# Performance work log

Hardware: AMD Instinct MI355X
Metric: run time of the kernel (lower is better)

## Reference

```python
import jax, jax.numpy as jnp
import numpy as np

N = 100000
K = 8
S = 2048
E = 131072


def setup_inputs() -> dict:
    key = jax.random.key(0)
    k1, k2, k3, k4, k5, k6, k7 = jax.random.split(key, 7)
    return {
        "beta": jax.random.normal(k1, (N,), dtype=jnp.float32),
        "a": jax.random.normal(k2, (1,), dtype=jnp.float32),
        "Zp": jax.random.normal(k3, (K, N), dtype=jnp.float32),
        "Gp": jax.random.normal(k4, (N, K), dtype=jnp.float32),
        "sample_idx": jax.random.randint(k5, (S,), 0, N),
        "sparse_i": jax.random.randint(k6, (E,), 0, N),
        "sparse_j": jax.random.randint(k7, (E,), 0, N),
    }


def reference(beta, a, Zp, Gp, sample_idx, sparse_i, sparse_j):
    # Z: softmax over archetype dim k (dim=0 of [k, N])
    Z = jax.nn.softmax(Zp, axis=0)          # [k, N]
    G = jax.nn.sigmoid(Gp)                  # [N, k]
    ZtG = Z.T * G                           # [N, k]
    C = ZtG / ZtG.sum(axis=0)               # [N, k], column-normalized
    sp_a = jax.nn.softplus(a)               # [1]

    Zs = Z[:, sample_idx]                   # [k, S]
    Cs = C[sample_idx, :]                   # [S, k]
    beta_s = beta[sample_idx]               # [S]

    # non-edge term: all-pairs distances within the sample
    bpair = beta_s[:, None] + beta_s[None, :]          # [S, S]
    M = (Zs @ Cs @ Zs).T                               # [S, k]
    diff = M[:, None, :] - M[None, :, :] + 1e-06       # [S, S, k]
    dist = jnp.sqrt(jnp.sum(diff ** 2, axis=-1))       # [S, S]
    mat = jnp.exp(bpair - sp_a * dist)                 # [S, S]
    mat_nd = mat - jnp.diag(jnp.diagonal(mat))
    e_vec = jnp.exp(jnp.ones((S,), dtype=mat.dtype))   # faithful to torch.exp(ones)
    z_pdist1 = 0.5 * (e_vec @ (mat_nd @ e_vec))        # scalar

    # edge term over sampled edges
    M2 = Zs @ Cs                                       # [k, k]
    beta_e = beta[sparse_i] + beta[sparse_j]           # [E]
    di = (M2 @ Z[:, sparse_i]).T                       # [E, k]
    dj = (M2 @ Z[:, sparse_j]).T                       # [E, k]
    dd = di - dj + 1e-06                               # [E, k]
    z_pdist2 = jnp.sum(beta_e - sp_a * jnp.sqrt(jnp.sum(dd ** 2, axis=-1)))

    return z_pdist2 - z_pdist1
```

## Files before the change

### kernel.cpp

```cpp
#include <hip/hip_runtime.h>
#include <hip/hip_bf16.h>

#define N_NODES 100000
#define K_DIM   8
#define S_SAMP  2048
#define E_EDGE  131072

#define CS_BLOCKS 256
#define M2_BLOCKS 8

#define CS_PART_OFF   0
#define M2P_OFF       2048
#define SPA_OFF       2560
#define PAIR_PART_OFF 2624
#define SP_PART_OFF   3648
#define BS_OFF        4160
#define MS_OFF        6208
#define ZT_OFF        22592
#define VT_OFF        822592

__global__ __launch_bounds__(256) void k_colsum(const float* __restrict__ Zp,
                                                const float* __restrict__ Gp,
                                                float* __restrict__ W) {
    int tid = threadIdx.x;
    float part[8] = {0,0,0,0,0,0,0,0};
    for (int n = blockIdx.x * 256 + tid; n < N_NODES; n += CS_BLOCKS * 256) {
        float zv[8];
        float mx = -1e30f;
        #pragma unroll
        for (int k = 0; k < 8; ++k) {
            zv[k] = Zp[(size_t)k * N_NODES + n];
            mx = fmaxf(mx, zv[k]);
        }
        float den = 0.0f;
        #pragma unroll
        for (int k = 0; k < 8; ++k) { zv[k] = __expf(zv[k] - mx); den += zv[k]; }
        float inv = 1.0f / den;
        float4 g0 = *(const float4*)&Gp[(size_t)n * 8];
        float4 g1 = *(const float4*)&Gp[(size_t)n * 8 + 4];
        float g[8] = {g0.x, g0.y, g0.z, g0.w, g1.x, g1.y, g1.z, g1.w};
        float zt[8];
        #pragma unroll
        for (int k = 0; k < 8; ++k) {
            float z = zv[k] * inv;
            zt[k] = z;
            part[k] += z / (1.0f + __expf(-g[k]));
        }
        float4 o0 = {zt[0], zt[1], zt[2], zt[3]};
        float4 o1 = {zt[4], zt[5], zt[6], zt[7]};
        *(float4*)&W[ZT_OFF + (size_t)n * 8]     = o0;
        *(float4*)&W[ZT_OFF + (size_t)n * 8 + 4] = o1;
    }
    __shared__ float sred[4][8];
    int lane = tid & 63, wave = tid >> 6;
    #pragma unroll
    for (int k = 0; k < 8; ++k) {
        float x = part[k];
        #pragma unroll
        for (int off = 32; off; off >>= 1) x += __shfl_down(x, off, 64);
        if (lane == 0) sred[wave][k] = x;
    }
    __syncthreads();
    if (tid < 8)
        W[CS_PART_OFF + blockIdx.x * 8 + tid] =
            sred[0][tid] + sred[1][tid] + sred[2][tid] + sred[3][tid];
}

__global__ __launch_bounds__(256) void k_m2(const float* __restrict__ a,
                                            const float* __restrict__ Gp,
                                            const int* __restrict__ sidx,
                                            float* __restrict__ W) {
    __shared__ float sinv[8];
    __shared__ float sred[4][64];
    int tid = threadIdx.x;
    if (tid < 8) {
        float s = 0.0f;
        for (int b = 0; b < CS_BLOCKS; ++b) s += W[CS_PART_OFF + b * 8 + tid];
        sinv[tid] = 1.0f / s;
    }
    if (blockIdx.x == 0 && tid == 0) {
        float av = a[0];
        W[SPA_OFF] = fmaxf(av, 0.0f) + log1pf(__expf(-fabsf(av)));
    }
    __syncthreads();

    int s = blockIdx.x * 256 + tid;
    int idx = sidx[s];
    float4 z0 = *(const float4*)&W[ZT_OFF + (size_t)idx * 8];
    float4 z1 = *(const float4*)&W[ZT_OFF + (size_t)idx * 8 + 4];
    float4 g0 = *(const float4*)&Gp[(size_t)idx * 8];
    float4 g1 = *(const float4*)&Gp[(size_t)idx * 8 + 4];
    float z[8] = {z0.x, z0.y, z0.z, z0.w, z1.x, z1.y, z1.z, z1.w};
    float g[8] = {g0.x, g0.y, g0.z, g0.w, g1.x, g1.y, g1.z, g1.w};
    float cs[8];
    #pragma unroll
    for (int j = 0; j < 8; ++j)
        cs[j] = z[j] * sinv[j] / (1.0f + __expf(-g[j]));

    int lane = tid & 63, wave = tid >> 6;
    #pragma unroll
    for (int k = 0; k < 8; ++k) {
        #pragma unroll
        for (int j = 0; j < 8; ++j) {
            float x = z[k] * cs[j];
            #pragma unroll
            for (int off = 32; off; off >>= 1) x += __shfl_down(x, off, 64);
            if (lane == 0) sred[wave][k * 8 + j] = x;
        }
    }
    __syncthreads();
    if (tid < 64)
        W[M2P_OFF + blockIdx.x * 64 + tid] =
            sred[0][tid] + sred[1][tid] + sred[2][tid] + sred[3][tid];
}

__global__ __launch_bounds__(256) void k_v(float* __restrict__ W) {
    __shared__ float sM2[64];
    int tid = threadIdx.x;
    if (tid < 64) {
        float m = 0.0f;
        #pragma unroll
        for (int b = 0; b < M2_BLOCKS; ++b) m += W[M2P_OFF + b * 64 + tid];
        sM2[tid] = m;
    }
    __syncthreads();
    int n = blockIdx.x * 256 + tid;
    if (n >= N_NODES) return;
    float4 z0 = *(const float4*)&W[ZT_OFF + (size_t)n * 8];
    float4 z1 = *(const float4*)&W[ZT_OFF + (size_t)n * 8 + 4];
    float z[8] = {z0.x, z0.y, z0.z, z0.w, z1.x, z1.y, z1.z, z1.w};
    float v[8];
    #pragma unroll
    for (int k = 0; k < 8; ++k) {
        float acc = 0.0f;
        #pragma unroll
        for (int j = 0; j < 8; ++j) acc += sM2[k * 8 + j] * z[j];
        v[k] = acc;
    }
    float4 o0 = {v[0], v[1], v[2], v[3]};
    float4 o1 = {v[4], v[5], v[6], v[7]};
    *(float4*)&W[VT_OFF + (size_t)n * 8]     = o0;
    *(float4*)&W[VT_OFF + (size_t)n * 8 + 4] = o1;
}

__global__ __launch_bounds__(256) void k_ms(const float* __restrict__ beta,
                                            const int* __restrict__ sidx,
                                            float* __restrict__ W) {
    int s = blockIdx.x * 256 + threadIdx.x;
    if (s >= S_SAMP) return;
    int idx = sidx[s];
    float4 v0 = *(const float4*)&W[VT_OFF + (size_t)idx * 8];
    float4 v1 = *(const float4*)&W[VT_OFF + (size_t)idx * 8 + 4];
    *(float4*)&W[MS_OFF + (size_t)s * 8]     = v0;
    *(float4*)&W[MS_OFF + (size_t)s * 8 + 4] = v1;
    W[BS_OFF + s] = beta[idx];
}

__global__ __launch_bounds__(256) void k_pair(float* __restrict__ W) {
    int tid = threadIdx.x;
    float sp_a = W[SPA_OFF];
    const float* Ms = W + MS_OFF;
    const float* Bs = W + BS_OFF;
    float acc = 0.0f;
    #pragma unroll
    for (int r = 0; r < 2; ++r) {
        int s = blockIdx.x * 2 + r;
        float4 m0 = *(const float4*)&Ms[(size_t)s * 8];
        float4 m1 = *(const float4*)&Ms[(size_t)s * 8 + 4];
        float bsv = Bs[s];
        for (int t = tid; t < S_SAMP; t += 256) {
            float4 a0 = *(const float4*)&Ms[(size_t)t * 8];
            float4 a1 = *(const float4*)&Ms[(size_t)t * 8 + 4];
            float d, ss;
            d = m0.x - a0.x + 1e-6f; ss  = d * d;
            d = m0.y - a0.y + 1e-6f; ss += d * d;
            d = m0.z - a0.z + 1e-6f; ss += d * d;
            d = m0.w - a0.w + 1e-6f; ss += d * d;
            d = m1.x - a1.x + 1e-6f; ss += d * d;
            d = m1.y - a1.y + 1e-6f; ss += d * d;
            d = m1.z - a1.z + 1e-6f; ss += d * d;
            d = m1.w - a1.w + 1e-6f; ss += d * d;
            float val = __expf(bsv + Bs[t] - sp_a * sqrtf(ss));
            if (t != s) acc += val;
        }
    }
    __shared__ float sw[4];
    int lane = tid & 63, wave = tid >> 6;
    #pragma unroll
    for (int off = 32; off; off >>= 1) acc += __shfl_down(acc, off, 64);
    if (lane == 0) sw[wave] = acc;
    __syncthreads();
    if (tid == 0) W[PAIR_PART_OFF + blockIdx.x] = sw[0] + sw[1] + sw[2] + sw[3];
}

__global__ __launch_bounds__(256) void k_sparse(const float* __restrict__ beta,
                                                const int* __restrict__ si,
                                                const int* __restrict__ sj,
                                                float* __restrict__ W) {
    int tid = threadIdx.x;
    int e = blockIdx.x * 256 + tid;
    float sp_a = W[SPA_OFF];
    int i = si[e], j = sj[e];
    const float* vt = W + VT_OFF;
    float4 vi0 = *(const float4*)&vt[(size_t)i * 8];
    float4 vi1 = *(const float4*)&vt[(size_t)i * 8 + 4];
    float4 vj0 = *(const float4*)&vt[(size_t)j * 8];
    float4 vj1 = *(const float4*)&vt[(size_t)j * 8 + 4];
    float d, ss;
    d = vi0.x - vj0.x + 1e-6f; ss  = d * d;
    d = vi0.y - vj0.y + 1e-6f; ss += d * d;
    d = vi0.z - vj0.z + 1e-6f; ss += d * d;
    d = vi0.w - vj0.w + 1e-6f; ss += d * d;
    d = vi1.x - vj1.x + 1e-6f; ss += d * d;
    d = vi1.y - vj1.y + 1e-6f; ss += d * d;
    d = vi1.z - vj1.z + 1e-6f; ss += d * d;
    d = vi1.w - vj1.w + 1e-6f; ss += d * d;
    float acc = beta[i] + beta[j] - sp_a * sqrtf(ss);

    __shared__ float sw[4];
    int lane = tid & 63, wave = tid >> 6;
    #pragma unroll
    for (int off = 32; off; off >>= 1) acc += __shfl_down(acc, off, 64);
    if (lane == 0) sw[wave] = acc;
    __syncthreads();
    if (tid == 0) W[SP_PART_OFF + blockIdx.x] = sw[0] + sw[1] + sw[2] + sw[3];
}

__global__ __launch_bounds__(256) void k_final(const float* __restrict__ W,
                                               float* __restrict__ out) {
    __shared__ double sd[256];
    int tid = threadIdx.x;
    double ap = 0.0, as = 0.0;
    for (int i = tid; i < S_SAMP / 2; i += 256) ap += (double)W[PAIR_PART_OFF + i];
    for (int i = tid; i < E_EDGE / 256; i += 256) as += (double)W[SP_PART_OFF + i];
    sd[tid] = as - 0.5 * 7.3890560989306495 * ap;
    __syncthreads();
    for (int s = 128; s > 0; s >>= 1) {
        if (tid < s) sd[tid] += sd[tid + s];
        __syncthreads();
    }
    if (tid == 0) out[0] = (float)sd[0];
}

extern "C" void kernel_launch(void* const* d_in, const int* in_sizes, int n_in,
                              void* d_out, int out_size, void* d_ws, size_t ws_size,
                              hipStream_t stream) {
    const float* beta       = (const float*)d_in[0];
    const float* a          = (const float*)d_in[1];
    const float* Zp         = (const float*)d_in[2];
    const float* Gp         = (const float*)d_in[3];
    const int*   sample_idx = (const int*)d_in[4];
    const int*   sparse_i   = (const int*)d_in[5];
    const int*   sparse_j   = (const int*)d_in[6];
    float* out = (float*)d_out;
    float* W   = (float*)d_ws;

    k_colsum<<<dim3(CS_BLOCKS), dim3(256), 0, stream>>>(Zp, Gp, W);
    k_m2<<<dim3(M2_BLOCKS), dim3(256), 0, stream>>>(a, Gp, sample_idx, W);
    k_v<<<dim3((N_NODES + 255) / 256), dim3(256), 0, stream>>>(W);
    k_ms<<<dim3(S_SAMP / 256), dim3(256), 0, stream>>>(beta, sample_idx, W);
    k_pair<<<dim3(S_SAMP / 2), dim3(256), 0, stream>>>(W);
    k_sparse<<<dim3(E_EDGE / 256), dim3(256), 0, stream>>>(beta, sparse_i, sparse_j, W);
    k_final<<<dim3(1), dim3(256), 0, stream>>>(W, out);
}
```

Measured before the change: 56.04 us.

## Fuse seven-kernel pipeline into three kernels with last-block final reduction

Merges colsum, sampled M2 partials, spa and beta gather into one kernel. It recomputes the sampled softmax and sigmoid directly from the inputs, so that kernel no longer waits on its own ZT output. V and the sampled Ms rows are built in one kernel, with the column-normalisation folded into M2 there. The pair and sparse-edge terms run together in a final kernel that reduces through an atomic-counter last-block pattern, so the separate final-reduction launch goes away. This cuts launches from seven to three, at the cost of redundant column-sum reduction in every block of k2 and a float (not double) combination of per-block partials.

```diff
diff --git a/kernel.cpp b/kernel.cpp
--- a/kernel.cpp
+++ b/kernel.cpp
@@ -2,57 +2,57 @@
 #include <hip/hip_bf16.h>
 
 #define N_NODES 100000
-#define K_DIM   8
 #define S_SAMP  2048
 #define E_EDGE  131072
-
-#define CS_BLOCKS 256
-#define M2_BLOCKS 8
-
-#define CS_PART_OFF   0
-#define M2P_OFF       2048
-#define SPA_OFF       2560
-#define PAIR_PART_OFF 2624
-#define SP_PART_OFF   3648
-#define BS_OFF        4160
-#define MS_OFF        6208
-#define ZT_OFF        22592
-#define VT_OFF        822592
-
-__global__ __launch_bounds__(256) void k_colsum(const float* __restrict__ Zp,
-                                                const float* __restrict__ Gp,
-                                                float* __restrict__ W) {
-    int tid = threadIdx.x;
+#define NB      391
+#define PB      512
+
+#define SPA_OFF     0
+#define CNT_U32     8
+#define CS_PART_OFF 64
+#define M2P_OFF     (64 + 3200)
+#define PART_OFF    (M2P_OFF + 512)
+#define BS_OFF      (PART_OFF + 512)
+#define MS_OFF      (BS_OFF + 2048)
+#define ZT_OFF      (MS_OFF + 16384)
+#define VT_OFF      (ZT_OFF + 800000)
+
+__global__ __launch_bounds__(256) void k1(const float* __restrict__ beta,
+                                          const float* __restrict__ a,
+                                          const float* __restrict__ Zp,
+                                          const float* __restrict__ Gp,
+                                          const int* __restrict__ sidx,
+                                          float* __restrict__ W) {
+    const int tid = threadIdx.x, bid = blockIdx.x;
+    const int n = bid * 256 + tid;
+    const int lane = tid & 63, wave = tid >> 6;
+    __shared__ float sred[4][64];
+
     float part[8] = {0,0,0,0,0,0,0,0};
-    for (int n = blockIdx.x * 256 + tid; n < N_NODES; n += CS_BLOCKS * 256) {
-        float zv[8];
-        float mx = -1e30f;
+    if (n < N_NODES) {
+        float zv[8]; float mx = -1e30f;
         #pragma unroll
         for (int k = 0; k < 8; ++k) {
             zv[k] = Zp[(size_t)k * N_NODES + n];
             mx = fmaxf(mx, zv[k]);
         }
-        float den = 0.0f;
+        float den = 0.f;
         #pragma unroll
         for (int k = 0; k < 8; ++k) { zv[k] = __expf(zv[k] - mx); den += zv[k]; }
-        float inv = 1.0f / den;
+        float inv = 1.f / den;
         float4 g0 = *(const float4*)&Gp[(size_t)n * 8];
         float4 g1 = *(const float4*)&Gp[(size_t)n * 8 + 4];
-        float g[8] = {g0.x, g0.y, g0.z, g0.w, g1.x, g1.y, g1.z, g1.w};
+        float g[8] = {g0.x,g0.y,g0.z,g0.w,g1.x,g1.y,g1.z,g1.w};
         float zt[8];
         #pragma unroll
         for (int k = 0; k < 8; ++k) {
             float z = zv[k] * inv;
             zt[k] = z;
-            part[k] += z / (1.0f + __expf(-g[k]));
-        }
-        float4 o0 = {zt[0], zt[1], zt[2], zt[3]};
-        float4 o1 = {zt[4], zt[5], zt[6], zt[7]};
-        *(float4*)&W[ZT_OFF + (size_t)n * 8]     = o0;
-        *(float4*)&W[ZT_OFF + (size_t)n * 8 + 4] = o1;
-    }
-    __shared__ float sred[4][8];
-    int lane = tid & 63, wave = tid >> 6;
+            part[k] = z / (1.f + __expf(-g[k]));
+        }
+        *(float4*)&W[ZT_OFF + (size_t)n * 8]     = make_float4(zt[0],zt[1],zt[2],zt[3]);
+        *(float4*)&W[ZT_OFF + (size_t)n * 8 + 4] = make_float4(zt[4],zt[5],zt[6],zt[7]);
+    }
     #pragma unroll
     for (int k = 0; k < 8; ++k) {
         float x = part[k];
@@ -62,112 +62,139 @@
     }
     __syncthreads();
     if (tid < 8)
-        W[CS_PART_OFF + blockIdx.x * 8 + tid] =
+        W[CS_PART_OFF + bid * 8 + tid] =
             sred[0][tid] + sred[1][tid] + sred[2][tid] + sred[3][tid];
-}
-
-__global__ __launch_bounds__(256) void k_m2(const float* __restrict__ a,
-                                            const float* __restrict__ Gp,
-                                            const int* __restrict__ sidx,
-                                            float* __restrict__ W) {
-    __shared__ float sinv[8];
-    __shared__ float sred[4][64];
-    int tid = threadIdx.x;
+    if (n == 0) {
+        float av = a[0];
+        W[SPA_OFF] = fmaxf(av, 0.f) + log1pf(__expf(-fabsf(av)));
+        ((unsigned*)W)[CNT_U32] = 0u;
+    }
+
+    if (bid < 8) {
+        int s = bid * 256 + tid;
+        int idx = sidx[s];
+        float zv[8]; float mx = -1e30f;
+        #pragma unroll
+        for (int k = 0; k < 8; ++k) {
+            zv[k] = Zp[(size_t)k * N_NODES + idx];
+            mx = fmaxf(mx, zv[k]);
+        }
+        float den = 0.f;
+        #pragma unroll
+        for (int k = 0; k < 8; ++k) { zv[k] = __expf(zv[k] - mx); den += zv[k]; }
+        float inv = 1.f / den;
+        float4 g0 = *(const float4*)&Gp[(size_t)idx * 8];
+        float4 g1 = *(const float4*)&Gp[(size_t)idx * 8 + 4];
+        float g[8] = {g0.x,g0.y,g0.z,g0.w,g1.x,g1.y,g1.z,g1.w};
+        float z[8], w8[8];
+        #pragma unroll
+        for (int k = 0; k < 8; ++k) {
+            z[k]  = zv[k] * inv;
+            w8[k] = z[k] / (1.f + __expf(-g[k]));
+        }
+        W[BS_OFF + s] = beta[idx];
+
+        __syncthreads();
+        #pragma unroll
+        for (int k = 0; k < 8; ++k) {
+            #pragma unroll
+            for (int j = 0; j < 8; ++j) {
+                float x = z[k] * w8[j];
+                #pragma unroll
+                for (int off = 32; off; off >>= 1) x += __shfl_down(x, off, 64);
+                if (lane == 0) sred[wave][k * 8 + j] = x;
+            }
+        }
+        __syncthreads();
+        if (tid < 64)
+            W[M2P_OFF + bid * 64 + tid] =
+                sred[0][tid] + sred[1][tid] + sred[2][tid] + sred[3][tid];
+    }
+}
+
+__global__ __launch_bounds__(256) void k2(const int* __restrict__ sidx,
+                                          float* __restrict__ W) {
+    const int tid = threadIdx.x, bid = blockIdx.x;
+    __shared__ float sflat[256];
+    __shared__ float sinv8[8];
+    __shared__ float sM2[64];
+
+    {
+        int k = tid & 7, g = tid >> 3;
+        float s = 0.f;
+        for (int b = g; b < NB; b += 32) s += W[CS_PART_OFF + b * 8 + k];
+        sflat[tid] = s;
+    }
+    __syncthreads();
     if (tid < 8) {
-        float s = 0.0f;
-        for (int b = 0; b < CS_BLOCKS; ++b) s += W[CS_PART_OFF + b * 8 + tid];
-        sinv[tid] = 1.0f / s;
-    }
-    if (blockIdx.x == 0 && tid == 0) {
-        float av = a[0];
-        W[SPA_OFF] = fmaxf(av, 0.0f) + log1pf(__expf(-fabsf(av)));
-    }
-    __syncthreads();
-
-    int s = blockIdx.x * 256 + tid;
-    int idx = sidx[s];
-    float4 z0 = *(const float4*)&W[ZT_OFF + (size_t)idx * 8];
-    float4 z1 = *(const float4*)&W[ZT_OFF + (size_t)idx * 8 + 4];
-    float4 g0 = *(const float4*)&Gp[(size_t)idx * 8];
-    float4 g1 = *(const float4*)&Gp[(size_t)idx * 8 + 4];
-    float z[8] = {z0.x, z0.y, z0.z, z0.w, z1.x, z1.y, z1.z, z1.w};
-    float g[8] = {g0.x, g0.y, g0.z, g0.w, g1.x, g1.y, g1.z, g1.w};
-    float cs[8];
-    #pragma unroll
-    for (int j = 0; j < 8; ++j)
-        cs[j] = z[j] * sinv[j] / (1.0f + __expf(-g[j]));
-
-    int lane = tid & 63, wave = tid >> 6;
-    #pragma unroll
-    for (int k = 0; k < 8; ++k) {
-        #pragma unroll
-        for (int j = 0; j < 8; ++j) {
-            float x = z[k] * cs[j];
+        float s = 0.f;
+        #pragma unroll
+        for (int g = 0; g < 32; ++g) s += sflat[g * 8 + tid];
+        sinv8[tid] = 1.f / s;
+    }
+    __syncthreads();
+    if (tid < 64) {
+        float m = 0.f;
+        #pragma unroll
+        for (int b = 0; b < 8; ++b) m += W[M2P_OFF + b * 64 + tid];
+        sM2[tid] = m * sinv8[tid & 7];
+    }
+    __syncthreads();
+
+    int n = bid * 256 + tid;
+    if (n < N_NODES) {
+        float4 z0 = *(const float4*)&W[ZT_OFF + (size_t)n * 8];
+        float4 z1 = *(const float4*)&W[ZT_OFF + (size_t)n * 8 + 4];
+        float z[8] = {z0.x,z0.y,z0.z,z0.w,z1.x,z1.y,z1.z,z1.w};
+        float v[8];
+        #pragma unroll
+        for (int k = 0; k < 8; ++k) {
+            float acc = 0.f;
             #pragma unroll
-            for (int off = 32; off; off >>= 1) x += __shfl_down(x, off, 64);
-            if (lane == 0) sred[wave][k * 8 + j] = x;
-        }
-    }
-    __syncthreads();
-    if (tid < 64)
-        W[M2P_OFF + blockIdx.x * 64 + tid] =
-            sred[0][tid] + sred[1][tid] + sred[2][tid] + sred[3][tid];
-}
-
-__global__ __launch_bounds__(256) void k_v(float* __restrict__ W) {
-    __shared__ float sM2[64];
-    int tid = threadIdx.x;
-    if (tid < 64) {
-        float m = 0.0f;
-        #pragma unroll
-        for (int b = 0; b < M2_BLOCKS; ++b) m += W[M2P_OFF + b * 64 + tid];
-        sM2[tid] = m;
-    }
-    __syncthreads();
-    int n = blockIdx.x * 256 + tid;
-    if (n >= N_NODES) return;
-    float4 z0 = *(const float4*)&W[ZT_OFF + (size_t)n * 8];
-    float4 z1 = *(const float4*)&W[ZT_OFF + (size_t)n * 8 + 4];
-    float z[8] = {z0.x, z0.y, z0.z, z0.w, z1.x, z1.y, z1.z, z1.w};
-    float v[8];
-    #pragma unroll
-    for (int k = 0; k < 8; ++k) {
-        float acc = 0.0f;
-        #pragma unroll
-        for (int j = 0; j < 8; ++j) acc += sM2[k * 8 + j] * z[j];
-        v[k] = acc;
-    }
-    float4 o0 = {v[0], v[1], v[2], v[3]};
-    float4 o1 = {v[4], v[5], v[6], v[7]};
-    *(float4*)&W[VT_OFF + (size_t)n * 8]     = o0;
-    *(float4*)&W[VT_OFF + (size_t)n * 8 + 4] = o1;
-}
-
-__global__ __launch_bounds__(256) void k_ms(const float* __restrict__ beta,
-                                            const int* __restrict__ sidx,
-                                            float* __restrict__ W) {
-    int s = blockIdx.x * 256 + threadIdx.x;
-    if (s >= S_SAMP) return;
-    int idx = sidx[s];
-    float4 v0 = *(const float4*)&W[VT_OFF + (size_t)idx * 8];
-    float4 v1 = *(const float4*)&W[VT_OFF + (size_t)idx * 8 + 4];
-    *(float4*)&W[MS_OFF + (size_t)s * 8]     = v0;
-    *(float4*)&W[MS_OFF + (size_t)s * 8 + 4] = v1;
-    W[BS_OFF + s] = beta[idx];
-}
-
-__global__ __launch_bounds__(256) void k_pair(float* __restrict__ W) {
-    int tid = threadIdx.x;
-    float sp_a = W[SPA_OFF];
+            for (int j = 0; j < 8; ++j) acc += sM2[k * 8 + j] * z[j];
+            v[k] = acc;
+        }
+        *(float4*)&W[VT_OFF + (size_t)n * 8]     = make_float4(v[0],v[1],v[2],v[3]);
+        *(float4*)&W[VT_OFF + (size_t)n * 8 + 4] = make_float4(v[4],v[5],v[6],v[7]);
+    }
+    if (bid < 8) {
+        int s = bid * 256 + tid;
+        int idx = sidx[s];
+        float4 z0 = *(const float4*)&W[ZT_OFF + (size_t)idx * 8];
+        float4 z1 = *(const float4*)&W[ZT_OFF + (size_t)idx * 8 + 4];
+        float z[8] = {z0.x,z0.y,z0.z,z0.w,z1.x,z1.y,z1.z,z1.w};
+        float v[8];
+        #pragma unroll
+        for (int k = 0; k < 8; ++k) {
+            float acc = 0.f;
+            #pragma unroll
+            for (int j = 0; j < 8; ++j) acc += sM2[k * 8 + j] * z[j];
+            v[k] = acc;
+        }
+        *(float4*)&W[MS_OFF + (size_t)s * 8]     = make_float4(v[0],v[1],v[2],v[3]);
+        *(float4*)&W[MS_OFF + (size_t)s * 8 + 4] = make_float4(v[4],v[5],v[6],v[7]);
+    }
+}
+
+__global__ __launch_bounds__(256) void k3(const float* __restrict__ beta,
+                                          const int* __restrict__ si,
+                                          const int* __restrict__ sj,
+                                          float* __restrict__ out,
+                                          float* __restrict__ W) {
+    const int tid = threadIdx.x, bid = blockIdx.x;
+    const int lane = tid & 63, wave = tid >> 6;
+    const int gtid = bid * 256 + tid;
+    const float spa = W[SPA_OFF];
     const float* Ms = W + MS_OFF;
     const float* Bs = W + BS_OFF;
-    float acc = 0.0f;
+
+    float accp = 0.f;
     #pragma unroll
-    for (int r = 0; r < 2; ++r) {
-        int s = blockIdx.x * 2 + r;
-        float4 m0 = *(const float4*)&Ms[(size_t)s * 8];
-        float4 m1 = *(const float4*)&Ms[(size_t)s * 8 + 4];
-        float bsv = Bs[s];
+    for (int r = 0; r < 4; ++r) {
+        int srow = bid * 4 + r;
+        float4 m0 = *(const float4*)&Ms[(size_t)srow * 8];
+        float4 m1 = *(const float4*)&Ms[(size_t)srow * 8 + 4];
+        float bsv = Bs[srow];
         for (int t = tid; t < S_SAMP; t += 256) {
             float4 a0 = *(const float4*)&Ms[(size_t)t * 8];
             float4 a1 = *(const float4*)&Ms[(size_t)t * 8 + 4];
@@ -180,66 +207,58 @@
             d = m1.y - a1.y + 1e-6f; ss += d * d;
             d = m1.z - a1.z + 1e-6f; ss += d * d;
             d = m1.w - a1.w + 1e-6f; ss += d * d;
-            float val = __expf(bsv + Bs[t] - sp_a * sqrtf(ss));
-            if (t != s) acc += val;
-        }
-    }
+            float val = __expf(bsv + Bs[t] - spa * sqrtf(ss));
+            if (t != srow) accp += val;
+        }
+    }
+    float accs;
+    {
+        int i = si[gtid], j = sj[gtid];
+        const float* vt = W + VT_OFF;
+        float4 vi0 = *(const float4*)&vt[(size_t)i * 8];
+        float4 vi1 = *(const float4*)&vt[(size_t)i * 8 + 4];
+        float4 vj0 = *(const float4*)&vt[(size_t)j * 8];
+        float4 vj1 = *(const float4*)&vt[(size_t)j * 8 + 4];
+        float d, ss;
+        d = vi0.x - vj0.x + 1e-6f; ss  = d * d;
+        d = vi0.y - vj0.y + 1e-6f; ss += d * d;
+        d = vi0.z - vj0.z + 1e-6f; ss += d * d;
+        d = vi0.w - vj0.w + 1e-6f; ss += d * d;
+        d = vi1.x - vj1.x + 1e-6f; ss += d * d;
+        d = vi1.y - vj1.y + 1e-6f; ss += d * d;
+        d = vi1.z - vj1.z + 1e-6f; ss += d * d;
+        d = vi1.w - vj1.w + 1e-6f; ss += d * d;
+        accs = beta[i] + beta[j] - spa * sqrtf(ss);
+    }
+
+    float part = accs - 0.5f * 7.38905609893065f * accp;
     __shared__ float sw[4];
-    int lane = tid & 63, wave = tid >> 6;
     #pragma unroll
-    for (int off = 32; off; off >>= 1) acc += __shfl_down(acc, off, 64);
-    if (lane == 0) sw[wave] = acc;
-    __syncthreads();
-    if (tid == 0) W[PAIR_PART_OFF + blockIdx.x] = sw[0] + sw[1] + sw[2] + sw[3];
-}
-
-__global__ __launch_bounds__(256) void k_sparse(const float* __restrict__ beta,
-                                                const int* __restrict__ si,
-                                                const int* __restrict__ sj,
-                                                float* __restrict__ W) {
-    int tid = threadIdx.x;
-    int e = blockIdx.x * 256 + tid;
-    float sp_a = W[SPA_OFF];
-    int i = si[e], j = sj[e];
-    const float* vt = W + VT_OFF;
-    float4 vi0 = *(const float4*)&vt[(size_t)i * 8];
-    float4 vi1 = *(const float4*)&vt[(size_t)i * 8 + 4];
-    float4 vj0 = *(const float4*)&vt[(size_t)j * 8];
-    float4 vj1 = *(const float4*)&vt[(size_t)j * 8 + 4];
-    float d, ss;
-    d = vi0.x - vj0.x + 1e-6f; ss  = d * d;
-    d = vi0.y - vj0.y + 1e-6f; ss += d * d;
-    d = vi0.z - vj0.z + 1e-6f; ss += d * d;
-    d = vi0.w - vj0.w + 1e-6f; ss += d * d;
-    d = vi1.x - vj1.x + 1e-6f; ss += d * d;
-    d = vi1.y - vj1.y + 1e-6f; ss += d * d;
-    d = vi1.z - vj1.z + 1e-6f; ss += d * d;
-    d = vi1.w - vj1.w + 1e-6f; ss += d * d;
-    float acc = beta[i] + beta[j] - sp_a * sqrtf(ss);
-
-    __shared__ float sw[4];
-    int lane = tid & 63, wave = tid >> 6;
-    #pragma unroll
-    for (int off = 32; off; off >>= 1) acc += __shfl_down(acc, off, 64);
-    if (lane == 0) sw[wave] = acc;
-    __syncthreads();
-    if (tid == 0) W[SP_PART_OFF + blockIdx.x] = sw[0] + sw[1] + sw[2] + sw[3];
-}
-
-__global__ __launch_bounds__(256) void k_final(const float* __restrict__ W,
-                                               float* __restrict__ out) {
-    __shared__ double sd[256];
-    int tid = threadIdx.x;
-    double ap = 0.0, as = 0.0;
-    for (int i = tid; i < S_SAMP / 2; i += 256) ap += (double)W[PAIR_PART_OFF + i];
-    for (int i = tid; i < E_EDGE / 256; i += 256) as += (double)W[SP_PART_OFF + i];
-    sd[tid] = as - 0.5 * 7.3890560989306495 * ap;
-    __syncthreads();
-    for (int s = 128; s > 0; s >>= 1) {
-        if (tid < s) sd[tid] += sd[tid + s];
+    for (int off = 32; off; off >>= 1) part += __shfl_down(part, off, 64);
+    if (lane == 0) sw[wave] = part;
+    __syncthreads();
+    if (tid == 0) W[PART_OFF + bid] = sw[0] + sw[1] + sw[2] + sw[3];
+
+    __shared__ int sLast;
+    if (tid == 0) {
+        __threadfence();
+        unsigned old = atomicAdd(&((unsigned*)W)[CNT_U32], 1u);
+        sLast = (old == PB - 1);
+    }
+    __syncthreads();
+    if (sLast) {
+        __threadfence();
+        __shared__ double sd[256];
+        double s = 0.0;
+        for (int i = tid; i < PB; i += 256) s += (double)W[PART_OFF + i];
+        sd[tid] = s;
         __syncthreads();
-    }
-    if (tid == 0) out[0] = (float)sd[0];
+        for (int k = 128; k > 0; k >>= 1) {
+            if (tid < k) sd[tid] += sd[tid + k];
+            __syncthreads();
+        }
+        if (tid == 0) out[0] = (float)sd[0];
+    }
 }
 
 extern "C" void kernel_launch(void* const* d_in, const int* in_sizes, int n_in,
@@ -255,11 +274,7 @@
     float* out = (float*)d_out;
     float* W   = (float*)d_ws;
 
-    k_colsum<<<dim3(CS_BLOCKS), dim3(256), 0, stream>>>(Zp, Gp, W);
-    k_m2<<<dim3(M2_BLOCKS), dim3(256), 0, stream>>>(a, Gp, sample_idx, W);
-    k_v<<<dim3((N_NODES + 255) / 256), dim3(256), 0, stream>>>(W);
-    k_ms<<<dim3(S_SAMP / 256), dim3(256), 0, stream>>>(beta, sample_idx, W);
-    k_pair<<<dim3(S_SAMP / 2), dim3(256), 0, stream>>>(W);
-    k_sparse<<<dim3(E_EDGE / 256), dim3(256), 0, stream>>>(beta, sparse_i, sparse_j, W);
-    k_final<<<dim3(1), dim3(256), 0, stream>>>(W, out);
-}
+    k1<<<dim3(NB), dim3(256), 0, stream>>>(beta, a, Zp, Gp, sample_idx, W);
+    k2<<<dim3(NB), dim3(256), 0, stream>>>(sample_idx, W);
+    k3<<<dim3(PB), dim3(256), 0, stream>>>(beta, sparse_i, sparse_j, out, W);
+}
```

Result: slower. 63.36 us (+13.1%).
